# Kernel tuning notes

Measured on AMD Instinct MI355X. Metric: run time of the kernel, lower is better.

The kernel has to match this reference:

```python
import jax, jax.numpy as jnp
import numpy as np

BANDS = [2,3,3,3,3,3,3,3,3,3,3,8,8,8,8,8,8,8,8,8,8,8,8,16,16,16,16,16,16,16,17]
C = 128      # channels
H = 512      # 4 * channels
MAXO = 17 * 12  # padded fc2 output dim (largest band)
EPS = 1e-5


def setup_inputs() -> dict:
    key = jax.random.key(0)
    k0, k1, k2, k3, k4 = jax.random.split(key, 5)
    B, T, K = 4, 2000, len(BANDS)
    x = jax.random.normal(k0, (B, C, T, K), jnp.float32)
    norm_w = jnp.ones((K, C), jnp.float32)
    norm_b = jnp.zeros((K, C), jnp.float32)
    fc1_w = jax.random.normal(k1, (K, H, C), jnp.float32) * 0.05
    fc1_b = jax.random.normal(k2, (K, H), jnp.float32) * 0.02
    fc2_w = jax.random.normal(k3, (K, MAXO, H), jnp.float32) * 0.05
    fc2_b = jax.random.normal(k4, (K, MAXO), jnp.float32) * 0.02
    return dict(x=x, norm_w=norm_w, norm_b=norm_b, fc1_w=fc1_w, fc1_b=fc1_b,
                fc2_w=fc2_w, fc2_b=fc2_b)


def reference(x, norm_w, norm_b, fc1_w, fc1_b, fc2_w, fc2_b):
    # x: [B, C, T, K]. GroupNorm(1, C) per band: normalize over (C, T), affine per channel.
    mean = jnp.mean(x, axis=(1, 2), keepdims=True)            # [B,1,1,K]
    var = jnp.var(x, axis=(1, 2), keepdims=True)
    xn = (x - mean) / jnp.sqrt(var + EPS)
    xn = xn * norm_w.T[None, :, None, :] + norm_b.T[None, :, None, :]
    # fc1 + tanh, batched over all bands (same shape per band, distinct weights)
    h = jnp.einsum('bctk,khc->btkh', xn, fc1_w) + fc1_b       # [B,T,K,H]
    h = jnp.tanh(h)
    # fc2 + GLU per band (heterogeneous output dims -> small fixed loop)
    outs = []
    for i, bw in enumerate(BANDS):
        o = h[:, :, i, :] @ fc2_w[i, :12 * bw].T + fc2_b[i, :12 * bw]  # [B,T,12*bw]
        a, g = jnp.split(o, 2, axis=-1)
        o = a * jax.nn.sigmoid(g)                             # GLU -> [B,T,6*bw]
        outs.append(o.reshape(o.shape[0], o.shape[1], bw, 3, 2))
    m = jnp.concatenate(outs, axis=2)                         # [B,T,257,3,2]
    return m.transpose(0, 2, 1, 3, 4)                         # [B,257,T,3,2]
```

## Files before the change

### kernel.cpp

```cpp
#include <hip/hip_runtime.h>
#include <hip/hip_bf16.h>

#define NBANDS 31
#define CDIM 128
#define TDIM 2000
#define HDIM 512
#define MTOT 8000
#define MAXO 204
#define OPAD 224
#define NMTILE 504
#define NMBK 63

typedef __attribute__((ext_vector_type(8))) short short8;
typedef __attribute__((ext_vector_type(4))) float f32x4;
typedef __attribute__((ext_vector_type(4))) unsigned int u32x4;
typedef __bf16 bf16x8 __attribute__((ext_vector_type(8)));

__constant__ int d_bw[NBANDS]   = {2,3,3,3,3,3,3,3,3,3,3,8,8,8,8,8,8,8,8,8,8,8,8,16,16,16,16,16,16,16,17};
__constant__ int d_boff[NBANDS] = {0,2,5,8,11,14,17,20,23,26,29,32,40,48,56,64,72,80,88,96,104,112,120,128,144,160,176,192,208,224,240};
__constant__ int d_nn16[NBANDS] = {2,3,3,3,3,3,3,3,3,3,3,6,6,6,6,6,6,6,6,6,6,6,6,12,12,12,12,12,12,12,13};

__device__ __forceinline__ unsigned short f2bf(float f) {
  unsigned int u = __float_as_uint(f);
  return (unsigned short)((u + 0x7fffu + ((u >> 16) & 1u)) >> 16);
}

__device__ __forceinline__ unsigned int cvt_pk_bf16(float lo, float hi) {
  unsigned int r;
  asm("v_cvt_pk_bf16_f32 %0, %1, %2" : "=v"(r) : "v"(lo), "v"(hi));
  return r;
}

__device__ __forceinline__ float fast_tanh(float x) {
  float p = __builtin_amdgcn_exp2f(2.885390082f * x);
  return 1.0f - 2.0f * __builtin_amdgcn_rcpf(p + 1.0f);
}

__device__ __forceinline__ float fast_sigmoid(float x) {
  return __builtin_amdgcn_rcpf(1.0f + __builtin_amdgcn_exp2f(-1.442695041f * x));
}

__device__ __forceinline__ f32x4 mfma_bf16(short8 a, short8 b, f32x4 c) {
  return __builtin_amdgcn_mfma_f32_16x16x32_bf16(
      __builtin_bit_cast(bf16x8, a), __builtin_bit_cast(bf16x8, b), c, 0, 0, 0);
}

__device__ __forceinline__ void g2lds(const char* gsrc, char* ldst, int lane) {
  __builtin_amdgcn_global_load_lds(
      (const __attribute__((address_space(1))) unsigned int*)(gsrc + lane * 16),
      (__attribute__((address_space(3))) unsigned int*)ldst, 16, 0, 0);
}

__launch_bounds__(256)
__global__ void k_pre(const float* __restrict__ x,
                      const float* __restrict__ norm_w, const float* __restrict__ norm_b,
                      const float* __restrict__ fc1_w, const float* __restrict__ fc1_b,
                      const float* __restrict__ fc2_w, const float* __restrict__ fc2_b,
                      unsigned short* __restrict__ xtf,
                      float* __restrict__ wsumP, float* __restrict__ wsqP,
                      unsigned short* __restrict__ w1f,
                      float* __restrict__ t1, float* __restrict__ t2,
                      unsigned short* __restrict__ w2f, float* __restrict__ b2) {
  __shared__ unsigned short tile[248 * 128];
  __shared__ float sred[256], sqred[256];
  const int bid = blockIdx.x;
  const int tid = threadIdx.x;

  if (bid < 1000) {
    const int tc = bid % 250, b = bid / 250;
    const int t0 = tc * 8;
    const float* p = x + ((size_t)b * CDIM * TDIM + t0) * NBANDS;
    const int cg = tid >> 6;
    const int f4 = tid & 63;
    if (f4 < 62) {
      const float* pf = p + f4 * 4;
      #pragma unroll 4
      for (int c2i = 0; c2i < 16; ++c2i) {
        const int c2 = cg * 16 + c2i;
        f32x4 va = *(const f32x4*)(pf + (size_t)c2 * 124000);
        f32x4 vb = *(const f32x4*)(pf + (size_t)c2 * 124000 + 62000);
        #pragma unroll
        for (int j = 0; j < 4; ++j) {
          const int f = f4 * 4 + j;
          *(unsigned int*)((char*)tile + f * 256 + ((4 * c2 + 4 * f) & 255)) =
              cvt_pk_bf16(va[j], vb[j]);
        }
      }
    }
    __syncthreads();
    float s = 0.f, sq = 0.f;
    if (tid < 248) {
      const char* row = (const char*)tile + tid * 256;
      const int st = 4 * tid;
      #pragma unroll 8
      for (int c2 = 0; c2 < 64; ++c2) {
        unsigned int u = *(const unsigned int*)(row + ((4 * c2 + st) & 255));
        float v0 = __uint_as_float(u << 16);
        float v1 = __uint_as_float(u & 0xffff0000u);
        s += v0 + v1;
        sq += v0 * v0 + v1 * v1;
      }
    }
    sred[tid] = s; sqred[tid] = sq;
    __syncthreads();
    if (tid < 31) {
      float ss = 0.f, qs = 0.f;
      #pragma unroll
      for (int j = 0; j < 8; ++j) { ss += sred[tid + 31 * j]; qs += sqred[tid + 31 * j]; }
      wsumP[((size_t)b * 250 + tc) * 31 + tid] = ss;
      wsqP [((size_t)b * 250 + tc) * 31 + tid] = qs;
    }
    for (int idx = tid; idx < 3968; idx += 256) {
      int ti = idx & 7, q4w = (idx >> 3) & 3, kkw = (idx >> 5) & 3, kb = idx >> 7;
      int f = ti * 31 + kb;
      const char* row = (const char*)tile + f * 256;
      const int st = 4 * f;
      u32x4 v;
      #pragma unroll
      for (int j = 0; j < 4; ++j)
        v[j] = *(const unsigned int*)(row + ((kkw * 64 + q4w * 16 + 4 * j + st) & 255));
      int m = b * TDIM + t0 + ti;
      int mtile = m >> 4, mrow = m & 15;
      size_t eoff = ((((size_t)kb * NMTILE + mtile) * 4 + kkw) * 64 + (mrow | (q4w << 4))) * 8;
      *(u32x4*)(xtf + eoff) = v;
    }
  } else if (bid < 1992) {
    const int idx = bid - 1000;
    const int c = tid & 127;
    const int hf2 = tid >> 7;
    #pragma unroll 1
    for (int it = 0; it < 8; ++it) {
      const int kn = idx * 16 + it * 2 + hf2;
      const int k = kn >> 9, n = kn & 511;
      float w  = fc1_w[(size_t)kn * CDIM + c];
      float nw = norm_w[k * CDIM + c];
      float nb = norm_b[k * CDIM + c];
      float wp = w * nw;
      {
        int nc = n >> 7, hh = (n >> 4) & 7, kk = c >> 5;
        int lnw = (n & 15) | (((c >> 3) & 3) << 4);
        size_t eoff = ((((size_t)(k * 4 + nc) * 8 + hh) * 4 + kk) * 64 + lnw) * 8 + (c & 7);
        w1f[eoff] = f2bf(wp);
      }
      float s1 = wp, s2 = w * nb;
      #pragma unroll
      for (int off = 32; off >= 1; off >>= 1) {
        s1 += __shfl_down(s1, off);
        s2 += __shfl_down(s2, off);
      }
      if ((tid & 63) == 0) { sred[tid >> 6] = s1; sqred[tid >> 6] = s2; }
      __syncthreads();
      if ((tid & 127) == 0) {
        t1[kn] = sred[hf2 * 2] + sred[hf2 * 2 + 1];
        t2[kn] = sqred[hf2 * 2] + sqred[hf2 * 2 + 1] + fc1_b[kn];
      }
      __syncthreads();
    }
  } else {
    const int idx = bid - 1992;
    #pragma unroll 1
    for (int oi = 0; oi < 8; ++oi) {
      const int ko = idx * 8 + oi;
      const int k = ko >> 8;
      const int o = ko & 255;
      const int bw = d_bw[k];
      const int O2 = 12 * bw, hf = 6 * bw;
      const bool valid = o < O2;
      const int srcrow = valid ? ((o & 1) ? (hf + (o >> 1)) : (o >> 1)) : 0;
      const float* sp = fc2_w + ((size_t)k * MAXO + srcrow) * HDIM;
      if (tid == 0 && o < OPAD)
        b2[k * OPAD + o] = valid ? fc2_b[k * MAXO + srcrow] : 0.f;
      const int ot = o >> 4, rr = o & 15;
      for (int j = tid; j < HDIM; j += 256) {
        int ks = j >> 5, hp = j & 31;
        int q  = (hp >> 2) & 3;
        int jj = ((hp >> 4) << 2) | (hp & 3);
        unsigned short val = valid ? f2bf(sp[j]) : (unsigned short)0;
        size_t eoff = (((size_t)(k * 16 + ks)) * 16 + ot) * 512 + (size_t)(rr | (q << 4)) * 8 + jj;
        w2f[eoff] = val;
      }
    }
  }
}

template<int SMAX, int NST>
__launch_bounds__(256, 2)
__global__ void k_gemm(const unsigned short* __restrict__ xtf,
                       const unsigned short* __restrict__ w1f,
                       const float* __restrict__ t1p, const float* __restrict__ t2p,
                       const unsigned short* __restrict__ w2f,
                       const float* __restrict__ b2p,
                       const float* __restrict__ wsumP, const float* __restrict__ wsqP,
                       float* __restrict__ out, int kbase, int nwg) {
  extern __shared__ char lds[];
  float* const t12 = (float*)lds;
  char* const B0 = lds + 4096;
  char* const B1 = B0 + NST * 1024;
  char* const B2 = B1 + NST * 1024;
  float* const sstat = (float*)(B2 + NST * 1024);
  float* const Ls  = (float*)lds;

  const int bid = blockIdx.x;
  const int qq = nwg >> 3, r8 = nwg & 7;
  const int xcd = bid & 7, ixd = bid >> 3;
  const int wg = (xcd < r8 ? xcd * (qq + 1) : r8 * (qq + 1) + (xcd - r8) * qq) + ixd;
  const int k = kbase + wg / NMBK;
  const int mb = wg - (k - kbase) * NMBK;
  const int m0 = mb * 128;

  const int tid = threadIdx.x;
  const int lane = tid & 63;
  const int wid = tid >> 6;
  const int col = lane & 15;
  const int q4 = lane >> 4;

  const int bw = d_bw[k];
  const int nn = d_nn16[k];
  const int half = 6 * bw;
  const int boffk = d_boff[k];

  const int b0 = m0 / 2000;
  const int b1 = ((m0 + 127 < MTOT) ? (m0 + 127) : (MTOT - 1)) / 2000;
  if (wid <= b1 - b0) {
    const int b = b0 + wid;
    float sP = 0.f, sQ = 0.f;
    for (int t = lane; t < 250; t += 64) {
      sP += wsumP[((size_t)b * 250 + t) * 31 + k];
      sQ += wsqP [((size_t)b * 250 + t) * 31 + k];
    }
    #pragma unroll
    for (int off = 32; off >= 1; off >>= 1) {
      sP += __shfl_down(sP, off);
      sQ += __shfl_down(sQ, off);
    }
    if (lane == 0) {
      const float n = (float)(CDIM * TDIM);
      float mean = sP / n;
      float var = sQ / n - mean * mean;
      sstat[wid * 2] = mean;
      sstat[wid * 2 + 1] = rsqrtf(var + 1e-5f);
    }
  }

  #pragma unroll
  for (int i = 0; i < 2; ++i) {
    t12[tid + i * 256] = t1p[k * HDIM + tid + i * 256];
    t12[512 + tid + i * 256] = t2p[k * HDIM + tid + i * 256];
  }

  const char* const w1kc = (const char*)w1f + (size_t)k * 131072;
  const char* const w2kc = (const char*)w2f + (size_t)k * 262144;

  auto stage = [&](char* buf, int c) {
    const char* w1c = w1kc + (((c >> 2) * 8 + (c & 3) * 2) * 4096);
    const char* w2c = w2kc + c * 16384;
    #pragma unroll
    for (int i = 0; i < NST / 4; ++i) {
      const int t = wid + i * 4;
      const char* src = (t < 8) ? (w1c + t * 1024) : (w2c + (t - 8) * 1024);
      g2lds(src, buf + t * 1024, lane);
    }
  };
  stage(B0, 0);

  const int mt0 = (m0 >> 4) + wid * 2;
  short8 xv[2][4];
  #pragma unroll
  for (int r = 0; r < 2; ++r)
    #pragma unroll
    for (int kk = 0; kk < 4; ++kk)
      xv[r][kk] = *(const short8*)(xtf +
          (((size_t)k * NMTILE + mt0 + r) * 4 + kk) * 512 + lane * 8);

  __syncthreads();

  float rs[2], rm[2];
  #pragma unroll
  for (int r = 0; r < 2; ++r) {
    int mr = m0 + wid * 32 + r * 16 + col;
    int mc = mr < (MTOT - 1) ? mr : (MTOT - 1);
    int bsel = mc / 2000 - b0;
    rs[r] = sstat[bsel * 2 + 1];
    rm[r] = rs[r] * sstat[bsel * 2];
  }

  const f32x4 fz = {0.f, 0.f, 0.f, 0.f};
  f32x4 acc2[SMAX][2];
  #pragma unroll
  for (int s = 0; s < SMAX; ++s) { acc2[s][0] = fz; acc2[s][1] = fz; }

  char* p0 = B0;
  char* p1 = B1;
  char* p2 = B2;

  #pragma unroll 1
  for (int c = 0; c < 16; ++c) {
    stage(p1, (c < 15) ? c + 1 : 15);
    if constexpr (NST == 24) asm volatile("s_waitcnt vmcnt(6)" ::: "memory");
    else if constexpr (NST == 16) asm volatile("s_waitcnt vmcnt(4)" ::: "memory");
    else asm volatile("s_waitcnt vmcnt(3)" ::: "memory");
    __builtin_amdgcn_s_barrier();
    __builtin_amdgcn_sched_barrier(0);

    char* const bc = p0;
    f32x4 a1[2][2];
    a1[0][0] = fz; a1[0][1] = fz; a1[1][0] = fz; a1[1][1] = fz;
    #pragma unroll
    for (int kk = 0; kk < 4; ++kk) {
      short8 wa0 = *(const short8*)(bc + kk * 1024 + lane * 16);
      short8 wa1 = *(const short8*)(bc + 4096 + kk * 1024 + lane * 16);
      #pragma unroll
      for (int r = 0; r < 2; ++r) {
        a1[0][r] = mfma_bf16(wa0, xv[r][kk], a1[0][r]);
        a1[1][r] = mfma_bf16(wa1, xv[r][kk], a1[1][r]);
      }
    }
    short8 hb[2];
    #pragma unroll
    for (int r = 0; r < 2; ++r) {
      u32x4 hbw;
      #pragma unroll
      for (int ht = 0; ht < 2; ++ht) {
        const f32x4 c1 = *(const f32x4*)(t12 + c * 32 + ht * 16 + q4 * 4);
        const f32x4 c2 = *(const f32x4*)(t12 + 512 + c * 32 + ht * 16 + q4 * 4);
        f32x4 v = a1[ht][r];
        float e0 = fast_tanh(fmaf(rs[r], v[0], fmaf(-rm[r], c1[0], c2[0])));
        float e1 = fast_tanh(fmaf(rs[r], v[1], fmaf(-rm[r], c1[1], c2[1])));
        float e2 = fast_tanh(fmaf(rs[r], v[2], fmaf(-rm[r], c1[2], c2[2])));
        float e3 = fast_tanh(fmaf(rs[r], v[3], fmaf(-rm[r], c1[3], c2[3])));
        hbw[ht * 2]     = cvt_pk_bf16(e0, e1);
        hbw[ht * 2 + 1] = cvt_pk_bf16(e2, e3);
      }
      hb[r] = __builtin_bit_cast(short8, hbw);
    }
    const char* w2l = bc + 8192;
    #pragma unroll
    for (int s = 0; s < SMAX; ++s) {
      if (s < nn) {
        short8 wb = *(const short8*)(w2l + s * 1024 + lane * 16);
        acc2[s][0] = mfma_bf16(wb, hb[0], acc2[s][0]);
        acc2[s][1] = mfma_bf16(wb, hb[1], acc2[s][1]);
      }
    }
    char* tmp = p0; p0 = p1; p1 = p2; p2 = tmp;
  }

  __syncthreads();

  const float* b2k = b2p + (size_t)k * OPAD;
  const bool plain = (m0 / 2000 == (m0 + 127) / 2000) && (m0 + 128 <= MTOT);
  if (plain) {
    #pragma unroll
    for (int s = 0; s < SMAX; ++s) {
      if (s < nn) {
        f32x4 bias = *(const f32x4*)(b2k + s * 16 + q4 * 4);
        #pragma unroll
        for (int r = 0; r < 2; ++r) {
          const int tloc = wid * 32 + r * 16 + col;
          f32x4 v = acc2[s][r];
          #pragma unroll
          for (int p = 0; p < 2; ++p) {
            float a = v[2 * p] + bias[2 * p];
            float g = v[2 * p + 1] + bias[2 * p + 1];
            int op = s * 8 + q4 * 2 + p;
            if (op < half) {
              int orr = op / 6, occ = op - orr * 6;
              Ls[(orr * 128 + tloc) * 6 + occ] = a * fast_sigmoid(g);
            }
          }
        }
      }
    }
    __syncthreads();
    const int bb = m0 / 2000;
    const int tb = m0 - bb * 2000;
    const size_t obase = ((size_t)bb * 257 + boffk) * 2000;
    const int tot = bw * 384;
    for (int ii = tid; ii < tot; ii += 256) {
      int orr = ii / 384;
      int rem = ii - orr * 384;
      *(unsigned long long*)(out + (obase + (size_t)orr * 2000 + tb) * 6 + rem * 2) =
          *(const unsigned long long*)(Ls + orr * 768 + rem * 2);
    }
  } else {
    #pragma unroll
    for (int s = 0; s < SMAX; ++s) {
      if (s < nn) {
        f32x4 bias = *(const f32x4*)(b2k + s * 16 + q4 * 4);
        #pragma unroll
        for (int r = 0; r < 2; ++r) {
          const int m = m0 + wid * 32 + r * 16 + col;
          f32x4 v = acc2[s][r];
          #pragma unroll
          for (int p = 0; p < 2; ++p) {
            float a = v[2 * p] + bias[2 * p];
            float g = v[2 * p + 1] + bias[2 * p + 1];
            int op = s * 8 + q4 * 2 + p;
            if (op < half && m < MTOT) {
              int bbm = m / 2000;
              int t = m - bbm * 2000;
              int orr = op / 6, occ = op - orr * 6;
              out[(((size_t)bbm * 257 + boffk + orr) * TDIM + t) * 6 + occ] =
                  a * fast_sigmoid(g);
            }
          }
        }
      }
    }
  }
}

extern "C" void kernel_launch(void* const* d_in, const int* in_sizes, int n_in,
                              void* d_out, int out_size, void* d_ws, size_t ws_size,
                              hipStream_t stream) {
  const float* x      = (const float*)d_in[0];
  const float* norm_w = (const float*)d_in[1];
  const float* norm_b = (const float*)d_in[2];
  const float* fc1_w  = (const float*)d_in[3];
  const float* fc1_b  = (const float*)d_in[4];
  const float* fc2_w  = (const float*)d_in[5];
  const float* fc2_b  = (const float*)d_in[6];
  float* out = (float*)d_out;
  char* ws = (char*)d_ws;

  size_t off = 0;
  float* wsumP = (float*)(ws + off); off += (size_t)4 * 250 * 31 * 4 + 128;
  float* wsqP  = (float*)(ws + off); off += (size_t)4 * 250 * 31 * 4 + 128;
  unsigned short* xtf = (unsigned short*)(ws + off); off += (size_t)NBANDS * NMTILE * 4 * 512 * 2;
  unsigned short* w1f = (unsigned short*)(ws + off); off += (size_t)NBANDS * 4 * 8 * 4 * 512 * 2;
  float* t1p = (float*)(ws + off); off += (size_t)NBANDS * HDIM * 4;
  float* t2p = (float*)(ws + off); off += (size_t)NBANDS * HDIM * 4;
  unsigned short* w2f = (unsigned short*)(ws + off); off += (size_t)NBANDS * 16 * 16 * 512 * 2;
  float* b2p = (float*)(ws + off); off += (size_t)NBANDS * OPAD * 4;

  hipLaunchKernelGGL(k_pre, dim3(2984), dim3(256), 0, stream,
                     x, norm_w, norm_b, fc1_w, fc1_b, fc2_w, fc2_b,
                     xtf, wsumP, wsqP, w1f, t1p, t2p, w2f, b2p);

  hipFuncSetAttribute((const void*)k_gemm<13,24>, hipFuncAttributeMaxDynamicSharedMemorySize, 77952);
  hipFuncSetAttribute((const void*)k_gemm<6,16>,  hipFuncAttributeMaxDynamicSharedMemorySize, 53376);
  hipFuncSetAttribute((const void*)k_gemm<3,12>,  hipFuncAttributeMaxDynamicSharedMemorySize, 41088);
  hipLaunchKernelGGL((k_gemm<13,24>), dim3(8 * NMBK),  dim3(256), 77952, stream,
                     xtf, w1f, t1p, t2p, w2f, b2p, wsumP, wsqP, out, 23, 8 * NMBK);
  hipLaunchKernelGGL((k_gemm<6,16>),  dim3(12 * NMBK), dim3(256), 53376, stream,
                     xtf, w1f, t1p, t2p, w2f, b2p, wsumP, wsqP, out, 11, 12 * NMBK);
  hipLaunchKernelGGL((k_gemm<3,12>),  dim3(11 * NMBK), dim3(256), 41088, stream,
                     xtf, w1f, t1p, t2p, w2f, b2p, wsumP, wsqP, out, 0,  11 * NMBK);
}
```

Baseline: 195.7 us.

## Split preprocessing blocks finer across channel halves and weight rows

The x-transpose/statistics blocks in k_pre now each handle half the channels, doubling that block count and halving the LDS tile, with a new rotation swizzle for bank-conflict avoidance. Weight-packing blocks process fewer rows each, giving many more blocks overall. Partial sums are stored per channel half, and the GEMM kernel reduces over twice as many partials. This aims to raise occupancy and parallelism in the preprocessing pass, at the cost of more blocks and a slightly larger statistics reduction.

```diff
diff --git a/kernel.cpp b/kernel.cpp
--- a/kernel.cpp
+++ b/kernel.cpp
@@ -49,6 +49,10 @@
   __builtin_amdgcn_global_load_lds(
       (const __attribute__((address_space(1))) unsigned int*)(gsrc + lane * 16),
       (__attribute__((address_space(3))) unsigned int*)ldst, 16, 0, 0);
+}
+
+__device__ __forceinline__ int rotf(int f) {
+  return ((f >> 2) + ((f & 3) << 3)) & 31;
 }
 
 __launch_bounds__(256)
@@ -61,28 +65,33 @@
                       unsigned short* __restrict__ w1f,
                       float* __restrict__ t1, float* __restrict__ t2,
                       unsigned short* __restrict__ w2f, float* __restrict__ b2) {
-  __shared__ unsigned short tile[248 * 128];
-  __shared__ float sred[256], sqred[256];
+  extern __shared__ char lds[];
+  unsigned short* const tile = (unsigned short*)lds;
+  float* const sred  = (float*)(lds + 31744);
+  float* const sqred = (float*)(lds + 32768);
   const int bid = blockIdx.x;
   const int tid = threadIdx.x;
 
-  if (bid < 1000) {
-    const int tc = bid % 250, b = bid / 250;
+  if (bid < 2000) {
+    const int chalf = bid & 1;
+    const int bt = bid >> 1;
+    const int tc = bt % 250, b = bt / 250;
     const int t0 = tc * 8;
     const float* p = x + ((size_t)b * CDIM * TDIM + t0) * NBANDS;
     const int cg = tid >> 6;
     const int f4 = tid & 63;
     if (f4 < 62) {
       const float* pf = p + f4 * 4;
-      #pragma unroll 4
-      for (int c2i = 0; c2i < 16; ++c2i) {
-        const int c2 = cg * 16 + c2i;
-        f32x4 va = *(const f32x4*)(pf + (size_t)c2 * 124000);
-        f32x4 vb = *(const f32x4*)(pf + (size_t)c2 * 124000 + 62000);
+      #pragma unroll
+      for (int c2i = 0; c2i < 8; ++c2i) {
+        const int c2l = cg * 8 + c2i;
+        const size_t cofs = (size_t)(chalf * 32 + c2l) * 124000;
+        f32x4 va = *(const f32x4*)(pf + cofs);
+        f32x4 vb = *(const f32x4*)(pf + cofs + 62000);
         #pragma unroll
         for (int j = 0; j < 4; ++j) {
           const int f = f4 * 4 + j;
-          *(unsigned int*)((char*)tile + f * 256 + ((4 * c2 + 4 * f) & 255)) =
+          *(unsigned int*)((char*)tile + f * 128 + ((4 * c2l + 4 * rotf(f)) & 127)) =
               cvt_pk_bf16(va[j], vb[j]);
         }
       }
@@ -90,11 +99,11 @@
     __syncthreads();
     float s = 0.f, sq = 0.f;
     if (tid < 248) {
-      const char* row = (const char*)tile + tid * 256;
-      const int st = 4 * tid;
+      const char* row = (const char*)tile + tid * 128;
+      const int st = 4 * rotf(tid);
       #pragma unroll 8
-      for (int c2 = 0; c2 < 64; ++c2) {
-        unsigned int u = *(const unsigned int*)(row + ((4 * c2 + st) & 255));
+      for (int c2 = 0; c2 < 32; ++c2) {
+        unsigned int u = *(const unsigned int*)(row + ((4 * c2 + st) & 127));
         float v0 = __uint_as_float(u << 16);
         float v1 = __uint_as_float(u & 0xffff0000u);
         s += v0 + v1;
@@ -107,30 +116,32 @@
       float ss = 0.f, qs = 0.f;
       #pragma unroll
       for (int j = 0; j < 8; ++j) { ss += sred[tid + 31 * j]; qs += sqred[tid + 31 * j]; }
-      wsumP[((size_t)b * 250 + tc) * 31 + tid] = ss;
-      wsqP [((size_t)b * 250 + tc) * 31 + tid] = qs;
-    }
-    for (int idx = tid; idx < 3968; idx += 256) {
-      int ti = idx & 7, q4w = (idx >> 3) & 3, kkw = (idx >> 5) & 3, kb = idx >> 7;
+      const size_t slot = (size_t)b * 500 + tc * 2 + chalf;
+      wsumP[slot * 31 + tid] = ss;
+      wsqP [slot * 31 + tid] = qs;
+    }
+    for (int idx = tid; idx < 1984; idx += 256) {
+      int ti = idx & 7, q4w = (idx >> 3) & 3, kkl = (idx >> 5) & 1, kb = idx >> 6;
       int f = ti * 31 + kb;
-      const char* row = (const char*)tile + f * 256;
-      const int st = 4 * f;
+      const char* row = (const char*)tile + f * 128;
+      const int st = 4 * rotf(f);
       u32x4 v;
       #pragma unroll
       for (int j = 0; j < 4; ++j)
-        v[j] = *(const unsigned int*)(row + ((kkw * 64 + q4w * 16 + 4 * j + st) & 255));
+        v[j] = *(const unsigned int*)(row + ((kkl * 64 + q4w * 16 + 4 * j + st) & 127));
       int m = b * TDIM + t0 + ti;
       int mtile = m >> 4, mrow = m & 15;
+      int kkw = chalf * 2 + kkl;
       size_t eoff = ((((size_t)kb * NMTILE + mtile) * 4 + kkw) * 64 + (mrow | (q4w << 4))) * 8;
       *(u32x4*)(xtf + eoff) = v;
     }
-  } else if (bid < 1992) {
-    const int idx = bid - 1000;
+  } else if (bid < 5968) {
+    const int idx = bid - 2000;
     const int c = tid & 127;
     const int hf2 = tid >> 7;
     #pragma unroll 1
-    for (int it = 0; it < 8; ++it) {
-      const int kn = idx * 16 + it * 2 + hf2;
+    for (int it = 0; it < 2; ++it) {
+      const int kn = idx * 4 + it * 2 + hf2;
       const int k = kn >> 9, n = kn & 511;
       float w  = fc1_w[(size_t)kn * CDIM + c];
       float nw = norm_w[k * CDIM + c];
@@ -157,10 +168,10 @@
       __syncthreads();
     }
   } else {
-    const int idx = bid - 1992;
+    const int idx = bid - 5968;
     #pragma unroll 1
-    for (int oi = 0; oi < 8; ++oi) {
-      const int ko = idx * 8 + oi;
+    for (int oi = 0; oi < 4; ++oi) {
+      const int ko = idx * 4 + oi;
       const int k = ko >> 8;
       const int o = ko & 255;
       const int bw = d_bw[k];
@@ -224,9 +235,9 @@
   if (wid <= b1 - b0) {
     const int b = b0 + wid;
     float sP = 0.f, sQ = 0.f;
-    for (int t = lane; t < 250; t += 64) {
-      sP += wsumP[((size_t)b * 250 + t) * 31 + k];
-      sQ += wsqP [((size_t)b * 250 + t) * 31 + k];
+    for (int t = lane; t < 500; t += 64) {
+      sP += wsumP[((size_t)b * 500 + t) * 31 + k];
+      sQ += wsqP [((size_t)b * 500 + t) * 31 + k];
     }
     #pragma unroll
     for (int off = 32; off >= 1; off >>= 1) {
@@ -424,8 +435,8 @@
   char* ws = (char*)d_ws;
 
   size_t off = 0;
-  float* wsumP = (float*)(ws + off); off += (size_t)4 * 250 * 31 * 4 + 128;
-  float* wsqP  = (float*)(ws + off); off += (size_t)4 * 250 * 31 * 4 + 128;
+  float* wsumP = (float*)(ws + off); off += (size_t)4 * 500 * 31 * 4 + 128;
+  float* wsqP  = (float*)(ws + off); off += (size_t)4 * 500 * 31 * 4 + 128;
   unsigned short* xtf = (unsigned short*)(ws + off); off += (size_t)NBANDS * NMTILE * 4 * 512 * 2;
   unsigned short* w1f = (unsigned short*)(ws + off); off += (size_t)NBANDS * 4 * 8 * 4 * 512 * 2;
   float* t1p = (float*)(ws + off); off += (size_t)NBANDS * HDIM * 4;
@@ -433,7 +444,8 @@
   unsigned short* w2f = (unsigned short*)(ws + off); off += (size_t)NBANDS * 16 * 16 * 512 * 2;
   float* b2p = (float*)(ws + off); off += (size_t)NBANDS * OPAD * 4;
 
-  hipLaunchKernelGGL(k_pre, dim3(2984), dim3(256), 0, stream,
+  hipFuncSetAttribute((const void*)k_pre, hipFuncAttributeMaxDynamicSharedMemorySize, 33792);
+  hipLaunchKernelGGL(k_pre, dim3(7952), dim3(256), 33792, stream,
                      x, norm_w, norm_b, fc1_w, fc1_b, fc2_w, fc2_b,
                      xtf, wsumP, wsqP, w1f, t1p, t2p, w2f, b2p);
 
```

Measured after the change: 173.6 us. 11.3% less time.
